# Optimization experiments

Measured on AMD Instinct MI355X. Metric: run time of the kernel, lower is better.

## Reference

```python
import jax, jax.numpy as jnp
import numpy as np

IN_SIZE = 128
HID = 256
N_SRC1 = 500000
N_DST1 = 100000
E1 = 1600000
N_DST2 = 16384
E2 = 262144


def setup_inputs() -> dict:
    key = jax.random.key(0)
    ks = jax.random.split(key, 12)
    x = jax.random.normal(ks[0], (N_SRC1, IN_SIZE), dtype=jnp.float32)
    src1 = jax.random.randint(ks[1], (E1,), 0, N_SRC1, dtype=jnp.int32)
    dst1 = jax.random.randint(ks[2], (E1,), 0, N_DST1, dtype=jnp.int32)
    src2 = jax.random.randint(ks[3], (E2,), 0, N_DST1, dtype=jnp.int32)
    dst2 = jax.random.randint(ks[4], (E2,), 0, N_DST2, dtype=jnp.int32)
    s_in = 1.0 / np.sqrt(IN_SIZE)
    s_h = 1.0 / np.sqrt(HID)
    W_self1 = jax.random.normal(ks[5], (IN_SIZE, HID), dtype=jnp.float32) * s_in
    W_neigh1 = jax.random.normal(ks[6], (IN_SIZE, HID), dtype=jnp.float32) * s_in
    b1 = jnp.zeros((HID,), dtype=jnp.float32)
    W_self2 = jax.random.normal(ks[7], (HID, HID), dtype=jnp.float32) * s_h
    W_neigh2 = jax.random.normal(ks[8], (HID, HID), dtype=jnp.float32) * s_h
    b2 = jnp.zeros((HID,), dtype=jnp.float32)
    return {
        "x": x,
        "src1": src1, "dst1": dst1,
        "src2": src2, "dst2": dst2,
        "W_self1": W_self1, "W_neigh1": W_neigh1, "b1": b1,
        "W_self2": W_self2, "W_neigh2": W_neigh2, "b2": b2,
        "n_dst1": N_DST1, "n_dst2": N_DST2,
    }


def sage_conv_mean(h, src, dst, n_dst, W_self, W_neigh, b):
    # DGL block convention: dst nodes are the first n_dst src nodes.
    # mean aggregation over incoming neighbors (zero-degree -> 0 via deg clamp)
    msg_sum = jax.ops.segment_sum(h[src], dst, num_segments=n_dst)  # [n_dst, d]
    deg = jax.ops.segment_sum(jnp.ones(src.shape, h.dtype), dst, num_segments=n_dst)
    h_neigh = msg_sum / jnp.maximum(deg, 1.0)[:, None]
    return h[:n_dst] @ W_self + h_neigh @ W_neigh + b


def reference(x, src1, dst1, src2, dst2,
              W_self1, W_neigh1, b1, W_self2, W_neigh2, b2,
              n_dst1, n_dst2):
    h = sage_conv_mean(x, src1, dst1, n_dst1, W_self1, W_neigh1, b1)
    h = jax.nn.relu(h)  # relu between layers only
    h = sage_conv_mean(h, src2, dst2, n_dst2, W_self2, W_neigh2, b2)
    return h
```

## Files before the change

kernel.cpp:

```cpp
#include <hip/hip_runtime.h>

#define IN_SIZE 128
#define HID 256
#define N_SRC1 500000
#define N_DST1 100000
#define E1 1600000
#define N_DST2 16384
#define E2 262144

#define NBIN1 196
#define NBIN2 32
#define P1B1  800
#define P1B2  256

#define OFF_XBF  0ull
#define OFF_H    76800000ull
#define OFF_MSG1 128000000ull
#define OFF_STG1 128000000ull
#define OFF_STG2 134400000ull
#define OFF_BP1  135448576ull
#define OFF_BP2  136075776ull
#define OFF_BT1  136108544ull
#define OFF_BT2  136109568ull
#define OFF_RPB1 136109824ull
#define OFF_RPB2 136110848ull
#define OFF_RP1  153600000ull
#define OFF_RP2  154000128ull
#define OFF_CSR1 154535424ull
#define OFF_CSR2 160935424ull
#define OFF_WP1  161984000ull
#define OFF_WP2  162115072ull

typedef __attribute__((ext_vector_type(8))) short short8;
typedef __attribute__((ext_vector_type(4))) float f32x4;

__device__ __forceinline__ unsigned short f2bf(float f) {
    unsigned u = __float_as_uint(f);
    return (unsigned short)((u + 0x7FFFu + ((u >> 16) & 1u)) >> 16);
}
__device__ __forceinline__ float bf2f(unsigned short b) {
    return __uint_as_float(((unsigned)b) << 16);
}

__global__ __launch_bounds__(256) void k_cast(
    const float* __restrict__ x, unsigned short* __restrict__ xbf)
{
    const int T = gridDim.x * 256;
    const int tid = blockIdx.x * 256 + threadIdx.x;
    const float4* x4 = (const float4*)x;
    short8* o8 = (short8*)xbf;
    for (int i = tid; i < N_SRC1 * IN_SIZE / 8; i += T) {
        const float4 u0 = x4[(size_t)i * 2];
        const float4 u1 = x4[(size_t)i * 2 + 1];
        short8 o;
        o[0] = (short)f2bf(u0.x); o[1] = (short)f2bf(u0.y);
        o[2] = (short)f2bf(u0.z); o[3] = (short)f2bf(u0.w);
        o[4] = (short)f2bf(u1.x); o[5] = (short)f2bf(u1.y);
        o[6] = (short)f2bf(u1.z); o[7] = (short)f2bf(u1.w);
        o8[i] = o;
    }
}

__global__ __launch_bounds__(256) void k_hist_bins(
    const int* __restrict__ dst1, int* __restrict__ hist1,
    const int* __restrict__ dst2, int* __restrict__ hist2)
{
    __shared__ int lcnt[NBIN1];
    const int tid = threadIdx.x;
    const bool l1 = blockIdx.x < P1B1;
    const int blk = l1 ? blockIdx.x : blockIdx.x - P1B1;
    const int nbins = l1 ? NBIN1 : NBIN2;
    const int chunk = l1 ? (E1 / P1B1) : (E2 / P1B2);
    const int* dst = l1 ? dst1 : dst2;
    int* hist = l1 ? hist1 : hist2;
    const int e0 = blk * chunk;
    for (int i = tid; i < nbins; i += 256) lcnt[i] = 0;
    __syncthreads();
    for (int i = tid; i < chunk; i += 256)
        atomicAdd(&lcnt[dst[e0 + i] >> 9], 1);
    __syncthreads();
    for (int i = tid; i < nbins; i += 256)
        hist[blk * nbins + i] = lcnt[i];
}

__global__ __launch_bounds__(256) void k_scan_offs(
    const int* __restrict__ hist1, int* __restrict__ blkpref1, int* __restrict__ bintot1,
    const int* __restrict__ hist2, int* __restrict__ blkpref2, int* __restrict__ bintot2)
{
    __shared__ int s[256];
    const int tid = threadIdx.x;
    const bool l1 = blockIdx.x < NBIN1;
    const int b = l1 ? blockIdx.x : blockIdx.x - NBIN1;
    const int nblk = l1 ? P1B1 : P1B2;
    const int nbins = l1 ? NBIN1 : NBIN2;
    const int* hist = l1 ? hist1 : hist2;
    int* blkpref = l1 ? blkpref1 : blkpref2;
    int* bintot = l1 ? bintot1 : bintot2;

    int v[4];
    int lsum = 0;
    #pragma unroll
    for (int j = 0; j < 4; ++j) {
        const int idx = tid * 4 + j;
        v[j] = (idx < nblk) ? hist[idx * nbins + b] : 0;
        lsum += v[j];
    }
    s[tid] = lsum;
    __syncthreads();
    for (int off = 1; off < 256; off <<= 1) {
        int t = (tid >= off) ? s[tid - off] : 0;
        __syncthreads();
        s[tid] += t;
        __syncthreads();
    }
    int run = s[tid] - lsum;
    #pragma unroll
    for (int j = 0; j < 4; ++j) {
        const int idx = tid * 4 + j;
        if (idx < nblk) blkpref[idx * nbins + b] = run;
        run += v[j];
    }
    if (tid == 255) bintot[b] = s[255];
}

__global__ __launch_bounds__(256) void k_binscan(
    const int* __restrict__ bt1, int* __restrict__ rpB1,
    const int* __restrict__ bt2, int* __restrict__ rpB2)
{
    __shared__ int s[256];
    const int tid = threadIdx.x;
    const bool l1 = (blockIdx.x == 0);
    const int n = l1 ? NBIN1 : NBIN2;
    const int* bt = l1 ? bt1 : bt2;
    int* rpB = l1 ? rpB1 : rpB2;
    const int v = (tid < n) ? bt[tid] : 0;
    s[tid] = v;
    __syncthreads();
    for (int off = 1; off < 256; off <<= 1) {
        int t = (tid >= off) ? s[tid - off] : 0;
        __syncthreads();
        s[tid] += t;
        __syncthreads();
    }
    if (tid < n) rpB[tid] = s[tid] - v;
    if (tid == n - 1) rpB[n] = s[tid];
}

__global__ __launch_bounds__(256) void k_place(
    const int* __restrict__ src1, const int* __restrict__ dst1,
    const int* __restrict__ blkpref1, const int* __restrict__ rpB1,
    unsigned* __restrict__ stg1,
    const int* __restrict__ src2, const int* __restrict__ dst2,
    const int* __restrict__ blkpref2, const int* __restrict__ rpB2,
    unsigned* __restrict__ stg2)
{
    __shared__ int lcur[NBIN1];
    const int tid = threadIdx.x;
    const bool l1 = blockIdx.x < P1B1;
    const int blk = l1 ? blockIdx.x : blockIdx.x - P1B1;
    const int nbins = l1 ? NBIN1 : NBIN2;
    const int chunk = l1 ? (E1 / P1B1) : (E2 / P1B2);
    const int* src = l1 ? src1 : src2;
    const int* dst = l1 ? dst1 : dst2;
    const int* blkpref = l1 ? blkpref1 : blkpref2;
    const int* rpB = l1 ? rpB1 : rpB2;
    unsigned* stg = l1 ? stg1 : stg2;
    const int e0 = blk * chunk;
    for (int i = tid; i < nbins; i += 256)
        lcur[i] = rpB[i] + blkpref[blk * nbins + i];
    __syncthreads();
    for (int i = tid; i < chunk; i += 256) {
        const int e = e0 + i;
        const int d = dst[e];
        const unsigned pk = ((unsigned)(d & 511) << 19) | (unsigned)src[e];
        const int pos = atomicAdd(&lcur[d >> 9], 1);
        stg[pos] = pk;
    }
}

__global__ __launch_bounds__(512) void k_fill_p2b(
    const unsigned* __restrict__ stg1, const int* __restrict__ rpB1,
    int* __restrict__ rp1, int* __restrict__ csr1,
    const unsigned* __restrict__ stg2, const int* __restrict__ rpB2,
    int* __restrict__ rp2, int* __restrict__ csr2)
{
    __shared__ int lcnt[512];
    __shared__ int s[512];
    const int tid = threadIdx.x;
    const bool l1 = blockIdx.x < NBIN1;
    const int b = l1 ? blockIdx.x : blockIdx.x - NBIN1;
    const int base = b << 9;
    const int ndst = l1 ? N_DST1 : N_DST2;
    const int nr = min(512, ndst - base);
    const unsigned* stg = l1 ? stg1 : stg2;
    const int* rpB = l1 ? rpB1 : rpB2;
    int* rp = l1 ? rp1 : rp2;
    int* csr = l1 ? csr1 : csr2;
    const int s0 = rpB[b], s1 = rpB[b + 1];

    lcnt[tid] = 0;
    __syncthreads();
    for (int i = s0 + tid; i < s1; i += 512)
        atomicAdd(&lcnt[stg[i] >> 19], 1);
    __syncthreads();

    const int v = lcnt[tid];
    s[tid] = v;
    __syncthreads();
    for (int off = 1; off < 512; off <<= 1) {
        int t = (tid >= off) ? s[tid - off] : 0;
        __syncthreads();
        s[tid] += t;
        __syncthreads();
    }
    const int excl = s0 + s[tid] - v;
    if (tid < nr) rp[base + tid] = excl;
    if (base + tid == ndst - 1) rp[ndst] = s1;
    __syncthreads();
    lcnt[tid] = excl;
    __syncthreads();

    for (int i = s0 + tid; i < s1; i += 512) {
        const unsigned pk = stg[i];
        const int pos = atomicAdd(&lcnt[pk >> 19], 1);
        csr[pos] = (int)(pk & 0x7FFFFu);
    }
}

__global__ __launch_bounds__(256) void k_pack(const float* __restrict__ Wa,
                                              const float* __restrict__ Wb,
                                              int Keach, unsigned short* __restrict__ out) {
    const int t = blockIdx.x * 256 + threadIdx.x;
    const int total = (2 * Keach / 32) * 1024;
    if (t >= total) return;
    const int kb = t >> 10;
    const int c  = (t >> 2) & 255;
    const int g  = t & 3;
    const int kbase = kb * 32 + g * 8;
    const float* W = (kbase < Keach) ? (Wa + (size_t)kbase * HID + c)
                                     : (Wb + (size_t)(kbase - Keach) * HID + c);
    unsigned short* o = out + ((size_t)kb * 256 + c) * 32 + g * 8;
    #pragma unroll
    for (int j = 0; j < 8; ++j) o[j] = f2bf(W[(size_t)j * HID]);
}

__global__ __launch_bounds__(256) void k_pull1(
    const unsigned short* __restrict__ xbf, const int* __restrict__ rp,
    const int* __restrict__ csr, unsigned short* __restrict__ msg)
{
    const int d = blockIdx.x * 8 + (threadIdx.x >> 5);
    const int hl = threadIdx.x & 31;
    const int beg = rp[d], end = rp[d + 1];
    float a0 = 0.f, a1 = 0.f, a2 = 0.f, a3 = 0.f;
    const unsigned short* xb = xbf + hl * 4;
    int j = beg;
    for (; j + 3 < end; j += 4) {
        const int s0 = csr[j], s1 = csr[j + 1], s2 = csr[j + 2], s3 = csr[j + 3];
        const uint2 va = *(const uint2*)(xb + (size_t)s0 * IN_SIZE);
        const uint2 vb = *(const uint2*)(xb + (size_t)s1 * IN_SIZE);
        const uint2 vc = *(const uint2*)(xb + (size_t)s2 * IN_SIZE);
        const uint2 vd = *(const uint2*)(xb + (size_t)s3 * IN_SIZE);
        a0 += (bf2f(va.x) + bf2f(vb.x)) + (bf2f(vc.x) + bf2f(vd.x));
        a1 += (bf2f(va.x >> 16) + bf2f(vb.x >> 16)) + (bf2f(vc.x >> 16) + bf2f(vd.x >> 16));
        a2 += (bf2f(va.y) + bf2f(vb.y)) + (bf2f(vc.y) + bf2f(vd.y));
        a3 += (bf2f(va.y >> 16) + bf2f(vb.y >> 16)) + (bf2f(vc.y >> 16) + bf2f(vd.y >> 16));
    }
    for (; j < end; ++j) {
        const uint2 va = *(const uint2*)(xb + (size_t)csr[j] * IN_SIZE);
        a0 += bf2f(va.x); a1 += bf2f(va.x >> 16);
        a2 += bf2f(va.y); a3 += bf2f(va.y >> 16);
    }
    const float inv = 1.0f / fmaxf((float)(end - beg), 1.0f);
    uint2 o;
    o.x = (unsigned)f2bf(a0 * inv) | ((unsigned)f2bf(a1 * inv) << 16);
    o.y = (unsigned)f2bf(a2 * inv) | ((unsigned)f2bf(a3 * inv) << 16);
    *(uint2*)(msg + (size_t)d * IN_SIZE + hl * 4) = o;
}

__global__ __launch_bounds__(256) void k_gemm1(
    const unsigned short* __restrict__ A1,
    const unsigned short* __restrict__ A2,
    const unsigned short* __restrict__ Wp,
    const float* __restrict__ bias,
    unsigned short* __restrict__ out)
{
    constexpr int NKS = 8;
    const int tid = threadIdx.x;
    const int wid = tid >> 6;
    const int lane = tid & 63;
    const int g = lane >> 4, r16 = lane & 15;
    const int i0 = blockIdx.x * 32;
    const int c0 = wid * 64;

    f32x4 acc[2][4];
    #pragma unroll
    for (int rb = 0; rb < 2; ++rb)
        #pragma unroll
        for (int cf = 0; cf < 4; ++cf)
            acc[rb][cf] = (f32x4){0.f, 0.f, 0.f, 0.f};

    #pragma unroll
    for (int ks = 0; ks < NKS; ++ks) {
        short8 a[2];
        #pragma unroll
        for (int rb = 0; rb < 2; ++rb) {
            const int row = i0 + rb * 16 + r16;
            const int kk = ks * 32 + g * 8;
            a[rb] = (ks < NKS / 2)
                ? *(const short8*)(A1 + (size_t)row * IN_SIZE + kk)
                : *(const short8*)(A2 + (size_t)row * IN_SIZE + (kk - IN_SIZE));
        }
        short8 b[4];
        #pragma unroll
        for (int cf = 0; cf < 4; ++cf) {
            const int col = c0 + cf * 16 + r16;
            b[cf] = *(const short8*)(Wp + ((size_t)ks * 256 + col) * 32 + g * 8);
        }
        #pragma unroll
        for (int rb = 0; rb < 2; ++rb)
            #pragma unroll
            for (int cf = 0; cf < 4; ++cf)
                acc[rb][cf] = __builtin_amdgcn_mfma_f32_16x16x32_bf16(
                    a[rb], b[cf], acc[rb][cf], 0, 0, 0);
    }

    #pragma unroll
    for (int cf = 0; cf < 4; ++cf) {
        const int col = c0 + cf * 16 + r16;
        const float bv = bias[col];
        #pragma unroll
        for (int rb = 0; rb < 2; ++rb)
            #pragma unroll
            for (int rr = 0; rr < 4; ++rr) {
                const int row = i0 + rb * 16 + g * 4 + rr;
                out[(size_t)row * HID + col] = f2bf(fmaxf(acc[rb][cf][rr] + bv, 0.0f));
            }
    }
}

__global__ __launch_bounds__(256) void k_sage2(
    const unsigned short* __restrict__ h,
    const int* __restrict__ rp, const int* __restrict__ csr,
    const unsigned short* __restrict__ Wp,
    const float* __restrict__ bias,
    float* __restrict__ out)
{
    __shared__ __align__(16) unsigned short At[32][264];
    const int tid = threadIdx.x;
    const int wid = tid >> 6;
    const int lane = tid & 63;
    const int i0 = blockIdx.x * 32;

    for (int r = 0; r < 8; ++r) {
        const int row = wid * 8 + r;
        const int d = i0 + row;
        const int beg = rp[d], end = rp[d + 1];
        float a0 = 0.f, a1 = 0.f, a2 = 0.f, a3 = 0.f;
        const unsigned short* hb = h + lane * 4;
        int j = beg;
        for (; j + 3 < end; j += 4) {
            const int s0 = csr[j], s1 = csr[j + 1], s2 = csr[j + 2], s3 = csr[j + 3];
            const uint2 va = *(const uint2*)(hb + (size_t)s0 * HID);
            const uint2 vb = *(const uint2*)(hb + (size_t)s1 * HID);
            const uint2 vc = *(const uint2*)(hb + (size_t)s2 * HID);
            const uint2 vd = *(const uint2*)(hb + (size_t)s3 * HID);
            a0 += (bf2f(va.x) + bf2f(vb.x)) + (bf2f(vc.x) + bf2f(vd.x));
            a1 += (bf2f(va.x >> 16) + bf2f(vb.x >> 16)) + (bf2f(vc.x >> 16) + bf2f(vd.x >> 16));
            a2 += (bf2f(va.y) + bf2f(vb.y)) + (bf2f(vc.y) + bf2f(vd.y));
            a3 += (bf2f(va.y >> 16) + bf2f(vb.y >> 16)) + (bf2f(vc.y >> 16) + bf2f(vd.y >> 16));
        }
        for (; j < end; ++j) {
            const uint2 va = *(const uint2*)(hb + (size_t)csr[j] * HID);
            a0 += bf2f(va.x); a1 += bf2f(va.x >> 16);
            a2 += bf2f(va.y); a3 += bf2f(va.y >> 16);
        }
        const float inv = 1.0f / fmaxf((float)(end - beg), 1.0f);
        uint2 o;
        o.x = (unsigned)f2bf(a0 * inv) | ((unsigned)f2bf(a1 * inv) << 16);
        o.y = (unsigned)f2bf(a2 * inv) | ((unsigned)f2bf(a3 * inv) << 16);
        *(uint2*)&At[row][lane * 4] = o;
    }
    __syncthreads();

    const int g = lane >> 4, r16 = lane & 15;
    const int c0 = wid * 64;
    f32x4 acc[2][4];
    #pragma unroll
    for (int rb = 0; rb < 2; ++rb)
        #pragma unroll
        for (int cf = 0; cf < 4; ++cf)
            acc[rb][cf] = (f32x4){0.f, 0.f, 0.f, 0.f};

    #pragma unroll
    for (int ks = 0; ks < 16; ++ks) {
        short8 a[2];
        #pragma unroll
        for (int rb = 0; rb < 2; ++rb) {
            const int row16 = rb * 16 + r16;
            if (ks < 8)
                a[rb] = *(const short8*)(h + (size_t)(i0 + row16) * HID + ks * 32 + g * 8);
            else
                a[rb] = *(const short8*)&At[row16][(ks - 8) * 32 + g * 8];
        }
        short8 b[4];
        #pragma unroll
        for (int cf = 0; cf < 4; ++cf) {
            const int col = c0 + cf * 16 + r16;
            b[cf] = *(const short8*)(Wp + ((size_t)ks * 256 + col) * 32 + g * 8);
        }
        #pragma unroll
        for (int rb = 0; rb < 2; ++rb)
            #pragma unroll
            for (int cf = 0; cf < 4; ++cf)
                acc[rb][cf] = __builtin_amdgcn_mfma_f32_16x16x32_bf16(
                    a[rb], b[cf], acc[rb][cf], 0, 0, 0);
    }

    #pragma unroll
    for (int cf = 0; cf < 4; ++cf) {
        const int col = c0 + cf * 16 + r16;
        const float bv = bias[col];
        #pragma unroll
        for (int rb = 0; rb < 2; ++rb)
            #pragma unroll
            for (int rr = 0; rr < 4; ++rr) {
                const int row = i0 + rb * 16 + g * 4 + rr;
                out[(size_t)row * HID + col] = acc[rb][cf][rr] + bv;
            }
    }
}

extern "C" void kernel_launch(void* const* d_in, const int* in_sizes, int n_in,
                              void* d_out, int out_size, void* d_ws, size_t ws_size,
                              hipStream_t stream) {
    const float* x       = (const float*)d_in[0];
    const int*   src1    = (const int*)d_in[1];
    const int*   dst1    = (const int*)d_in[2];
    const int*   src2    = (const int*)d_in[3];
    const int*   dst2    = (const int*)d_in[4];
    const float* W_self1 = (const float*)d_in[5];
    const float* W_neigh1= (const float*)d_in[6];
    const float* b1      = (const float*)d_in[7];
    const float* W_self2 = (const float*)d_in[8];
    const float* W_neigh2= (const float*)d_in[9];
    const float* b2      = (const float*)d_in[10];
    float* out = (float*)d_out;

    char* ws = (char*)d_ws;
    unsigned short* xbf  = (unsigned short*)(ws + OFF_XBF);
    unsigned short* h    = (unsigned short*)(ws + OFF_H);
    unsigned short* msg1 = (unsigned short*)(ws + OFF_MSG1);
    unsigned* stg1 = (unsigned*)(ws + OFF_STG1);
    unsigned* stg2 = (unsigned*)(ws + OFF_STG2);
    int* bp1  = (int*)(ws + OFF_BP1);
    int* bp2  = (int*)(ws + OFF_BP2);
    int* bt1  = (int*)(ws + OFF_BT1);
    int* bt2  = (int*)(ws + OFF_BT2);
    int* rpB1 = (int*)(ws + OFF_RPB1);
    int* rpB2 = (int*)(ws + OFF_RPB2);
    int* rp1  = (int*)(ws + OFF_RP1);
    int* rp2  = (int*)(ws + OFF_RP2);
    int* csr1 = (int*)(ws + OFF_CSR1);
    int* csr2 = (int*)(ws + OFF_CSR2);
    unsigned short* wp1 = (unsigned short*)(ws + OFF_WP1);
    unsigned short* wp2 = (unsigned short*)(ws + OFF_WP2);

    k_cast<<<2048, 256, 0, stream>>>(x, xbf);
    k_pack<<<32, 256, 0, stream>>>(W_self1, W_neigh1, 128, wp1);
    k_pack<<<64, 256, 0, stream>>>(W_self2, W_neigh2, 256, wp2);

    k_hist_bins<<<P1B1 + P1B2, 256, 0, stream>>>(dst1, bp1 , dst2, bp2);
    k_scan_offs<<<NBIN1 + NBIN2, 256, 0, stream>>>(bp1, bp1, bt1, bp2, bp2, bt2);
    k_binscan<<<2, 256, 0, stream>>>(bt1, rpB1, bt2, rpB2);
    k_place<<<P1B1 + P1B2, 256, 0, stream>>>(src1, dst1, bp1, rpB1, stg1,
                                             src2, dst2, bp2, rpB2, stg2);
    k_fill_p2b<<<NBIN1 + NBIN2, 512, 0, stream>>>(stg1, rpB1, rp1, csr1,
                                                  stg2, rpB2, rp2, csr2);

    k_pull1<<<N_DST1 / 8, 256, 0, stream>>>(xbf, rp1, csr1, msg1);
    k_gemm1<<<N_DST1 / 32, 256, 0, stream>>>(xbf, msg1, wp1, b1, h);
    k_sage2<<<N_DST2 / 32, 256, 0, stream>>>(h, rp2, csr2, wp2, b2, out);
}
```

Baseline: 313.6 us.

## Fuse layer-1 gather with GEMM and merge setup kernels

Layer-1 neighbor aggregation now runs inside the GEMM kernel: each block gathers mean messages for its 32 rows into shared memory and feeds them straight into the MFMA loop, so the msg1 buffer is never written to or read back from global memory. The cast and histogram kernels are merged into one launch, and the two weight-pack launches become one, which cuts launch overhead. The gather now uses a full wave per row with 4-byte loads and an 8-way unroll. Each GEMM block does 8 serial row gathers per wave before any matrix work, which may lower occupancy and reduce overlap between memory and compute.

```diff
diff --git a/kernel.cpp b/kernel.cpp
--- a/kernel.cpp
+++ b/kernel.cpp
@@ -14,22 +14,21 @@
 #define P1B2  256
 
 #define OFF_XBF  0ull
-#define OFF_H    76800000ull
-#define OFF_MSG1 128000000ull
-#define OFF_STG1 128000000ull
-#define OFF_STG2 134400000ull
-#define OFF_BP1  135448576ull
-#define OFF_BP2  136075776ull
-#define OFF_BT1  136108544ull
-#define OFF_BT2  136109568ull
-#define OFF_RPB1 136109824ull
-#define OFF_RPB2 136110848ull
-#define OFF_RP1  153600000ull
-#define OFF_RP2  154000128ull
-#define OFF_CSR1 154535424ull
-#define OFF_CSR2 160935424ull
-#define OFF_WP1  161984000ull
-#define OFF_WP2  162115072ull
+#define OFF_H    128000000ull
+#define OFF_STG1 179200000ull
+#define OFF_STG2 185600000ull
+#define OFF_BP1  186648576ull
+#define OFF_BP2  187275776ull
+#define OFF_BT1  187308544ull
+#define OFF_BT2  187309568ull
+#define OFF_RPB1 187310592ull
+#define OFF_RPB2 187311616ull
+#define OFF_RP1  187312640ull
+#define OFF_RP2  187712768ull
+#define OFF_CSR1 187778432ull
+#define OFF_CSR2 194178432ull
+#define OFF_WP1  195227008ull
+#define OFF_WP2  195358080ull
 
 typedef __attribute__((ext_vector_type(8))) short short8;
 typedef __attribute__((ext_vector_type(4))) float f32x4;
@@ -42,14 +41,37 @@
     return __uint_as_float(((unsigned)b) << 16);
 }
 
-__global__ __launch_bounds__(256) void k_cast(
-    const float* __restrict__ x, unsigned short* __restrict__ xbf)
-{
+__global__ __launch_bounds__(256) void k_cast_hist(
+    const float* __restrict__ x, unsigned short* __restrict__ xbf,
+    const int* __restrict__ dst1, int* __restrict__ hist1,
+    const int* __restrict__ dst2, int* __restrict__ hist2)
+{
+    __shared__ int lcnt[NBIN1];
+    const int bid = blockIdx.x;
+    const int tid = threadIdx.x;
+
+    if (bid < P1B1 + P1B2) {
+        const bool l1 = bid < P1B1;
+        const int blk = l1 ? bid : bid - P1B1;
+        const int nbins = l1 ? NBIN1 : NBIN2;
+        const int chunk = l1 ? (E1 / P1B1) : (E2 / P1B2);
+        const int* dst = l1 ? dst1 : dst2;
+        int* hist = l1 ? hist1 : hist2;
+        const int e0 = blk * chunk;
+        for (int i = tid; i < nbins; i += 256) lcnt[i] = 0;
+        __syncthreads();
+        for (int i = tid; i < chunk; i += 256)
+            atomicAdd(&lcnt[dst[e0 + i] >> 9], 1);
+        __syncthreads();
+        for (int i = tid; i < nbins; i += 256)
+            hist[blk * nbins + i] = lcnt[i];
+    }
+
     const int T = gridDim.x * 256;
-    const int tid = blockIdx.x * 256 + threadIdx.x;
+    const int gtid = bid * 256 + tid;
     const float4* x4 = (const float4*)x;
     short8* o8 = (short8*)xbf;
-    for (int i = tid; i < N_SRC1 * IN_SIZE / 8; i += T) {
+    for (int i = gtid; i < N_SRC1 * IN_SIZE / 8; i += T) {
         const float4 u0 = x4[(size_t)i * 2];
         const float4 u1 = x4[(size_t)i * 2 + 1];
         short8 o;
@@ -59,28 +81,6 @@
         o[6] = (short)f2bf(u1.z); o[7] = (short)f2bf(u1.w);
         o8[i] = o;
     }
-}
-
-__global__ __launch_bounds__(256) void k_hist_bins(
-    const int* __restrict__ dst1, int* __restrict__ hist1,
-    const int* __restrict__ dst2, int* __restrict__ hist2)
-{
-    __shared__ int lcnt[NBIN1];
-    const int tid = threadIdx.x;
-    const bool l1 = blockIdx.x < P1B1;
-    const int blk = l1 ? blockIdx.x : blockIdx.x - P1B1;
-    const int nbins = l1 ? NBIN1 : NBIN2;
-    const int chunk = l1 ? (E1 / P1B1) : (E2 / P1B2);
-    const int* dst = l1 ? dst1 : dst2;
-    int* hist = l1 ? hist1 : hist2;
-    const int e0 = blk * chunk;
-    for (int i = tid; i < nbins; i += 256) lcnt[i] = 0;
-    __syncthreads();
-    for (int i = tid; i < chunk; i += 256)
-        atomicAdd(&lcnt[dst[e0 + i] >> 9], 1);
-    __syncthreads();
-    for (int i = tid; i < nbins; i += 256)
-        hist[blk * nbins + i] = lcnt[i];
 }
 
 __global__ __launch_bounds__(256) void k_scan_offs(
@@ -227,12 +227,18 @@
     }
 }
 
-__global__ __launch_bounds__(256) void k_pack(const float* __restrict__ Wa,
-                                              const float* __restrict__ Wb,
-                                              int Keach, unsigned short* __restrict__ out) {
-    const int t = blockIdx.x * 256 + threadIdx.x;
-    const int total = (2 * Keach / 32) * 1024;
-    if (t >= total) return;
+__global__ __launch_bounds__(256) void k_pack2(
+    const float* __restrict__ Ws1, const float* __restrict__ Wn1,
+    unsigned short* __restrict__ wp1,
+    const float* __restrict__ Ws2, const float* __restrict__ Wn2,
+    unsigned short* __restrict__ wp2)
+{
+    const bool l1 = blockIdx.x < 32;
+    const int Keach = l1 ? 128 : 256;
+    const float* Wa = l1 ? Ws1 : Ws2;
+    const float* Wb = l1 ? Wn1 : Wn2;
+    unsigned short* out = l1 ? wp1 : wp2;
+    const int t = (l1 ? blockIdx.x : blockIdx.x - 32) * 256 + threadIdx.x;
     const int kb = t >> 10;
     const int c  = (t >> 2) & 255;
     const int g  = t & 3;
@@ -244,54 +250,50 @@
     for (int j = 0; j < 8; ++j) o[j] = f2bf(W[(size_t)j * HID]);
 }
 
-__global__ __launch_bounds__(256) void k_pull1(
+__global__ __launch_bounds__(256) void k_sage1(
     const unsigned short* __restrict__ xbf, const int* __restrict__ rp,
-    const int* __restrict__ csr, unsigned short* __restrict__ msg)
-{
-    const int d = blockIdx.x * 8 + (threadIdx.x >> 5);
-    const int hl = threadIdx.x & 31;
-    const int beg = rp[d], end = rp[d + 1];
-    float a0 = 0.f, a1 = 0.f, a2 = 0.f, a3 = 0.f;
-    const unsigned short* xb = xbf + hl * 4;
-    int j = beg;
-    for (; j + 3 < end; j += 4) {
-        const int s0 = csr[j], s1 = csr[j + 1], s2 = csr[j + 2], s3 = csr[j + 3];
-        const uint2 va = *(const uint2*)(xb + (size_t)s0 * IN_SIZE);
-        const uint2 vb = *(const uint2*)(xb + (size_t)s1 * IN_SIZE);
-        const uint2 vc = *(const uint2*)(xb + (size_t)s2 * IN_SIZE);
-        const uint2 vd = *(const uint2*)(xb + (size_t)s3 * IN_SIZE);
-        a0 += (bf2f(va.x) + bf2f(vb.x)) + (bf2f(vc.x) + bf2f(vd.x));
-        a1 += (bf2f(va.x >> 16) + bf2f(vb.x >> 16)) + (bf2f(vc.x >> 16) + bf2f(vd.x >> 16));
-        a2 += (bf2f(va.y) + bf2f(vb.y)) + (bf2f(vc.y) + bf2f(vd.y));
-        a3 += (bf2f(va.y >> 16) + bf2f(vb.y >> 16)) + (bf2f(vc.y >> 16) + bf2f(vd.y >> 16));
-    }
-    for (; j < end; ++j) {
-        const uint2 va = *(const uint2*)(xb + (size_t)csr[j] * IN_SIZE);
-        a0 += bf2f(va.x); a1 += bf2f(va.x >> 16);
-        a2 += bf2f(va.y); a3 += bf2f(va.y >> 16);
-    }
-    const float inv = 1.0f / fmaxf((float)(end - beg), 1.0f);
-    uint2 o;
-    o.x = (unsigned)f2bf(a0 * inv) | ((unsigned)f2bf(a1 * inv) << 16);
-    o.y = (unsigned)f2bf(a2 * inv) | ((unsigned)f2bf(a3 * inv) << 16);
-    *(uint2*)(msg + (size_t)d * IN_SIZE + hl * 4) = o;
-}
-
-__global__ __launch_bounds__(256) void k_gemm1(
-    const unsigned short* __restrict__ A1,
-    const unsigned short* __restrict__ A2,
-    const unsigned short* __restrict__ Wp,
-    const float* __restrict__ bias,
-    unsigned short* __restrict__ out)
-{
-    constexpr int NKS = 8;
+    const int* __restrict__ csr, const unsigned short* __restrict__ Wp,
+    const float* __restrict__ bias, unsigned short* __restrict__ outh)
+{
+    __shared__ __align__(16) unsigned short At[32][136];
     const int tid = threadIdx.x;
     const int wid = tid >> 6;
     const int lane = tid & 63;
+    const int i0 = blockIdx.x * 32;
+
+    for (int r = 0; r < 8; ++r) {
+        const int row = wid * 8 + r;
+        const int d = i0 + row;
+        const int beg = rp[d], end = rp[d + 1];
+        float a0 = 0.f, a1 = 0.f;
+        const unsigned short* xb = xbf + lane * 2;
+        int j = beg;
+        for (; j + 7 < end; j += 8) {
+            const unsigned v0 = *(const unsigned*)(xb + (size_t)csr[j + 0] * IN_SIZE);
+            const unsigned v1 = *(const unsigned*)(xb + (size_t)csr[j + 1] * IN_SIZE);
+            const unsigned v2 = *(const unsigned*)(xb + (size_t)csr[j + 2] * IN_SIZE);
+            const unsigned v3 = *(const unsigned*)(xb + (size_t)csr[j + 3] * IN_SIZE);
+            const unsigned v4 = *(const unsigned*)(xb + (size_t)csr[j + 4] * IN_SIZE);
+            const unsigned v5 = *(const unsigned*)(xb + (size_t)csr[j + 5] * IN_SIZE);
+            const unsigned v6 = *(const unsigned*)(xb + (size_t)csr[j + 6] * IN_SIZE);
+            const unsigned v7 = *(const unsigned*)(xb + (size_t)csr[j + 7] * IN_SIZE);
+            a0 += ((bf2f(v0) + bf2f(v1)) + (bf2f(v2) + bf2f(v3)))
+                + ((bf2f(v4) + bf2f(v5)) + (bf2f(v6) + bf2f(v7)));
+            a1 += ((bf2f(v0 >> 16) + bf2f(v1 >> 16)) + (bf2f(v2 >> 16) + bf2f(v3 >> 16)))
+                + ((bf2f(v4 >> 16) + bf2f(v5 >> 16)) + (bf2f(v6 >> 16) + bf2f(v7 >> 16)));
+        }
+        for (; j < end; ++j) {
+            const unsigned v = *(const unsigned*)(xb + (size_t)csr[j] * IN_SIZE);
+            a0 += bf2f(v); a1 += bf2f(v >> 16);
+        }
+        const float inv = 1.0f / fmaxf((float)(end - beg), 1.0f);
+        *(unsigned*)&At[row][lane * 2] =
+            (unsigned)f2bf(a0 * inv) | ((unsigned)f2bf(a1 * inv) << 16);
+    }
+    __syncthreads();
+
     const int g = lane >> 4, r16 = lane & 15;
-    const int i0 = blockIdx.x * 32;
     const int c0 = wid * 64;
-
     f32x4 acc[2][4];
     #pragma unroll
     for (int rb = 0; rb < 2; ++rb)
@@ -300,15 +302,15 @@
             acc[rb][cf] = (f32x4){0.f, 0.f, 0.f, 0.f};
 
     #pragma unroll
-    for (int ks = 0; ks < NKS; ++ks) {
+    for (int ks = 0; ks < 8; ++ks) {
         short8 a[2];
         #pragma unroll
         for (int rb = 0; rb < 2; ++rb) {
-            const int row = i0 + rb * 16 + r16;
-            const int kk = ks * 32 + g * 8;
-            a[rb] = (ks < NKS / 2)
-                ? *(const short8*)(A1 + (size_t)row * IN_SIZE + kk)
-                : *(const short8*)(A2 + (size_t)row * IN_SIZE + (kk - IN_SIZE));
+            const int row16 = rb * 16 + r16;
+            if (ks < 4)
+                a[rb] = *(const short8*)(xbf + (size_t)(i0 + row16) * IN_SIZE + ks * 32 + g * 8);
+            else
+                a[rb] = *(const short8*)&At[row16][(ks - 4) * 32 + g * 8];
         }
         short8 b[4];
         #pragma unroll
@@ -333,7 +335,7 @@
             #pragma unroll
             for (int rr = 0; rr < 4; ++rr) {
                 const int row = i0 + rb * 16 + g * 4 + rr;
-                out[(size_t)row * HID + col] = f2bf(fmaxf(acc[rb][cf][rr] + bv, 0.0f));
+                outh[(size_t)row * HID + col] = f2bf(fmaxf(acc[rb][cf][rr] + bv, 0.0f));
             }
     }
 }
@@ -359,11 +361,10 @@
         const unsigned short* hb = h + lane * 4;
         int j = beg;
         for (; j + 3 < end; j += 4) {
-            const int s0 = csr[j], s1 = csr[j + 1], s2 = csr[j + 2], s3 = csr[j + 3];
-            const uint2 va = *(const uint2*)(hb + (size_t)s0 * HID);
-            const uint2 vb = *(const uint2*)(hb + (size_t)s1 * HID);
-            const uint2 vc = *(const uint2*)(hb + (size_t)s2 * HID);
-            const uint2 vd = *(const uint2*)(hb + (size_t)s3 * HID);
+            const uint2 va = *(const uint2*)(hb + (size_t)csr[j + 0] * HID);
+            const uint2 vb = *(const uint2*)(hb + (size_t)csr[j + 1] * HID);
+            const uint2 vc = *(const uint2*)(hb + (size_t)csr[j + 2] * HID);
+            const uint2 vd = *(const uint2*)(hb + (size_t)csr[j + 3] * HID);
             a0 += (bf2f(va.x) + bf2f(vb.x)) + (bf2f(vc.x) + bf2f(vd.x));
             a1 += (bf2f(va.x >> 16) + bf2f(vb.x >> 16)) + (bf2f(vc.x >> 16) + bf2f(vd.x >> 16));
             a2 += (bf2f(va.y) + bf2f(vb.y)) + (bf2f(vc.y) + bf2f(vd.y));
@@ -447,9 +448,8 @@
     float* out = (float*)d_out;
 
     char* ws = (char*)d_ws;
-    unsigned short* xbf  = (unsigned short*)(ws + OFF_XBF);
-    unsigned short* h    = (unsigned short*)(ws + OFF_H);
-    unsigned short* msg1 = (unsigned short*)(ws + OFF_MSG1);
+    unsigned short* xbf = (unsigned short*)(ws + OFF_XBF);
+    unsigned short* h   = (unsigned short*)(ws + OFF_H);
     unsigned* stg1 = (unsigned*)(ws + OFF_STG1);
     unsigned* stg2 = (unsigned*)(ws + OFF_STG2);
     int* bp1  = (int*)(ws + OFF_BP1);
@@ -465,11 +465,9 @@
     unsigned short* wp1 = (unsigned short*)(ws + OFF_WP1);
     unsigned short* wp2 = (unsigned short*)(ws + OFF_WP2);
 
-    k_cast<<<2048, 256, 0, stream>>>(x, xbf);
-    k_pack<<<32, 256, 0, stream>>>(W_self1, W_neigh1, 128, wp1);
-    k_pack<<<64, 256, 0, stream>>>(W_self2, W_neigh2, 256, wp2);
-
-    k_hist_bins<<<P1B1 + P1B2, 256, 0, stream>>>(dst1, bp1 , dst2, bp2);
+    k_cast_hist<<<2048, 256, 0, stream>>>(x, xbf, dst1, bp1, dst2, bp2);
+    k_pack2<<<96, 256, 0, stream>>>(W_self1, W_neigh1, wp1, W_self2, W_neigh2, wp2);
+
     k_scan_offs<<<NBIN1 + NBIN2, 256, 0, stream>>>(bp1, bp1, bt1, bp2, bp2, bt2);
     k_binscan<<<2, 256, 0, stream>>>(bt1, rpB1, bt2, rpB2);
     k_place<<<P1B1 + P1B2, 256, 0, stream>>>(src1, dst1, bp1, rpB1, stg1,
@@ -477,7 +475,6 @@
     k_fill_p2b<<<NBIN1 + NBIN2, 512, 0, stream>>>(stg1, rpB1, rp1, csr1,
                                                   stg2, rpB2, rp2, csr2);
 
-    k_pull1<<<N_DST1 / 8, 256, 0, stream>>>(xbf, rp1, csr1, msg1);
-    k_gemm1<<<N_DST1 / 32, 256, 0, stream>>>(xbf, msg1, wp1, b1, h);
+    k_sage1<<<N_DST1 / 32, 256, 0, stream>>>(xbf, rp1, csr1, wp1, b1, h);
     k_sage2<<<N_DST2 / 32, 256, 0, stream>>>(h, rp2, csr2, wp2, b2, out);
 }
```

Result: slower. 333.1 us (+6.2%).

## Fuse cast with histogram, merge weight packs, unroll layer-1 gather by eight

Applied to the files above, without the earlier changes.

Merges the bf16 cast kernel with the destination histogram kernel, and the two weight-pack launches into one, to cut launch count and let the independent work overlap within one grid. The layer-1 neighbour gather loop is unrolled to eight rows per iteration so more loads are in flight. The workspace layout is reshuffled so the cast output no longer aliases buffers that the histogram now writes concurrently. The costs are higher register pressure in the pull kernel and more imbalance across blocks in the fused launch.

```diff
diff --git a/kernel.cpp b/kernel.cpp
--- a/kernel.cpp
+++ b/kernel.cpp
@@ -14,22 +14,22 @@
 #define P1B2  256
 
 #define OFF_XBF  0ull
-#define OFF_H    76800000ull
-#define OFF_MSG1 128000000ull
-#define OFF_STG1 128000000ull
-#define OFF_STG2 134400000ull
-#define OFF_BP1  135448576ull
-#define OFF_BP2  136075776ull
-#define OFF_BT1  136108544ull
-#define OFF_BT2  136109568ull
-#define OFF_RPB1 136109824ull
-#define OFF_RPB2 136110848ull
-#define OFF_RP1  153600000ull
-#define OFF_RP2  154000128ull
-#define OFF_CSR1 154535424ull
-#define OFF_CSR2 160935424ull
-#define OFF_WP1  161984000ull
-#define OFF_WP2  162115072ull
+#define OFF_H    128000000ull
+#define OFF_MSG1 179200000ull
+#define OFF_STG1 204800000ull
+#define OFF_STG2 211200000ull
+#define OFF_BP1  212248576ull
+#define OFF_BP2  212875776ull
+#define OFF_BT1  212908544ull
+#define OFF_BT2  212909568ull
+#define OFF_RPB1 212910592ull
+#define OFF_RPB2 212911616ull
+#define OFF_RP1  212912640ull
+#define OFF_RP2  213312768ull
+#define OFF_CSR1 213378432ull
+#define OFF_CSR2 219778432ull
+#define OFF_WP1  220827008ull
+#define OFF_WP2  220958080ull
 
 typedef __attribute__((ext_vector_type(8))) short short8;
 typedef __attribute__((ext_vector_type(4))) float f32x4;
@@ -42,14 +42,37 @@
     return __uint_as_float(((unsigned)b) << 16);
 }
 
-__global__ __launch_bounds__(256) void k_cast(
-    const float* __restrict__ x, unsigned short* __restrict__ xbf)
-{
+__global__ __launch_bounds__(256) void k_cast_hist(
+    const float* __restrict__ x, unsigned short* __restrict__ xbf,
+    const int* __restrict__ dst1, int* __restrict__ hist1,
+    const int* __restrict__ dst2, int* __restrict__ hist2)
+{
+    __shared__ int lcnt[NBIN1];
+    const int bid = blockIdx.x;
+    const int tid = threadIdx.x;
+
+    if (bid < P1B1 + P1B2) {
+        const bool l1 = bid < P1B1;
+        const int blk = l1 ? bid : bid - P1B1;
+        const int nbins = l1 ? NBIN1 : NBIN2;
+        const int chunk = l1 ? (E1 / P1B1) : (E2 / P1B2);
+        const int* dst = l1 ? dst1 : dst2;
+        int* hist = l1 ? hist1 : hist2;
+        const int e0 = blk * chunk;
+        for (int i = tid; i < nbins; i += 256) lcnt[i] = 0;
+        __syncthreads();
+        for (int i = tid; i < chunk; i += 256)
+            atomicAdd(&lcnt[dst[e0 + i] >> 9], 1);
+        __syncthreads();
+        for (int i = tid; i < nbins; i += 256)
+            hist[blk * nbins + i] = lcnt[i];
+    }
+
     const int T = gridDim.x * 256;
-    const int tid = blockIdx.x * 256 + threadIdx.x;
+    const int gtid = bid * 256 + tid;
     const float4* x4 = (const float4*)x;
     short8* o8 = (short8*)xbf;
-    for (int i = tid; i < N_SRC1 * IN_SIZE / 8; i += T) {
+    for (int i = gtid; i < N_SRC1 * IN_SIZE / 8; i += T) {
         const float4 u0 = x4[(size_t)i * 2];
         const float4 u1 = x4[(size_t)i * 2 + 1];
         short8 o;
@@ -59,28 +82,6 @@
         o[6] = (short)f2bf(u1.z); o[7] = (short)f2bf(u1.w);
         o8[i] = o;
     }
-}
-
-__global__ __launch_bounds__(256) void k_hist_bins(
-    const int* __restrict__ dst1, int* __restrict__ hist1,
-    const int* __restrict__ dst2, int* __restrict__ hist2)
-{
-    __shared__ int lcnt[NBIN1];
-    const int tid = threadIdx.x;
-    const bool l1 = blockIdx.x < P1B1;
-    const int blk = l1 ? blockIdx.x : blockIdx.x - P1B1;
-    const int nbins = l1 ? NBIN1 : NBIN2;
-    const int chunk = l1 ? (E1 / P1B1) : (E2 / P1B2);
-    const int* dst = l1 ? dst1 : dst2;
-    int* hist = l1 ? hist1 : hist2;
-    const int e0 = blk * chunk;
-    for (int i = tid; i < nbins; i += 256) lcnt[i] = 0;
-    __syncthreads();
-    for (int i = tid; i < chunk; i += 256)
-        atomicAdd(&lcnt[dst[e0 + i] >> 9], 1);
-    __syncthreads();
-    for (int i = tid; i < nbins; i += 256)
-        hist[blk * nbins + i] = lcnt[i];
 }
 
 __global__ __launch_bounds__(256) void k_scan_offs(
@@ -227,12 +228,18 @@
     }
 }
 
-__global__ __launch_bounds__(256) void k_pack(const float* __restrict__ Wa,
-                                              const float* __restrict__ Wb,
-                                              int Keach, unsigned short* __restrict__ out) {
-    const int t = blockIdx.x * 256 + threadIdx.x;
-    const int total = (2 * Keach / 32) * 1024;
-    if (t >= total) return;
+__global__ __launch_bounds__(256) void k_pack2(
+    const float* __restrict__ Ws1, const float* __restrict__ Wn1,
+    unsigned short* __restrict__ wp1,
+    const float* __restrict__ Ws2, const float* __restrict__ Wn2,
+    unsigned short* __restrict__ wp2)
+{
+    const bool l1 = blockIdx.x < 32;
+    const int Keach = l1 ? 128 : 256;
+    const float* Wa = l1 ? Ws1 : Ws2;
+    const float* Wb = l1 ? Wn1 : Wn2;
+    unsigned short* out = l1 ? wp1 : wp2;
+    const int t = (l1 ? blockIdx.x : blockIdx.x - 32) * 256 + threadIdx.x;
     const int kb = t >> 10;
     const int c  = (t >> 2) & 255;
     const int g  = t & 3;
@@ -254,16 +261,23 @@
     float a0 = 0.f, a1 = 0.f, a2 = 0.f, a3 = 0.f;
     const unsigned short* xb = xbf + hl * 4;
     int j = beg;
-    for (; j + 3 < end; j += 4) {
-        const int s0 = csr[j], s1 = csr[j + 1], s2 = csr[j + 2], s3 = csr[j + 3];
-        const uint2 va = *(const uint2*)(xb + (size_t)s0 * IN_SIZE);
-        const uint2 vb = *(const uint2*)(xb + (size_t)s1 * IN_SIZE);
-        const uint2 vc = *(const uint2*)(xb + (size_t)s2 * IN_SIZE);
-        const uint2 vd = *(const uint2*)(xb + (size_t)s3 * IN_SIZE);
-        a0 += (bf2f(va.x) + bf2f(vb.x)) + (bf2f(vc.x) + bf2f(vd.x));
-        a1 += (bf2f(va.x >> 16) + bf2f(vb.x >> 16)) + (bf2f(vc.x >> 16) + bf2f(vd.x >> 16));
-        a2 += (bf2f(va.y) + bf2f(vb.y)) + (bf2f(vc.y) + bf2f(vd.y));
-        a3 += (bf2f(va.y >> 16) + bf2f(vb.y >> 16)) + (bf2f(vc.y >> 16) + bf2f(vd.y >> 16));
+    for (; j + 7 < end; j += 8) {
+        const uint2 v0 = *(const uint2*)(xb + (size_t)csr[j + 0] * IN_SIZE);
+        const uint2 v1 = *(const uint2*)(xb + (size_t)csr[j + 1] * IN_SIZE);
+        const uint2 v2 = *(const uint2*)(xb + (size_t)csr[j + 2] * IN_SIZE);
+        const uint2 v3 = *(const uint2*)(xb + (size_t)csr[j + 3] * IN_SIZE);
+        const uint2 v4 = *(const uint2*)(xb + (size_t)csr[j + 4] * IN_SIZE);
+        const uint2 v5 = *(const uint2*)(xb + (size_t)csr[j + 5] * IN_SIZE);
+        const uint2 v6 = *(const uint2*)(xb + (size_t)csr[j + 6] * IN_SIZE);
+        const uint2 v7 = *(const uint2*)(xb + (size_t)csr[j + 7] * IN_SIZE);
+        a0 += ((bf2f(v0.x) + bf2f(v1.x)) + (bf2f(v2.x) + bf2f(v3.x)))
+            + ((bf2f(v4.x) + bf2f(v5.x)) + (bf2f(v6.x) + bf2f(v7.x)));
+        a1 += ((bf2f(v0.x >> 16) + bf2f(v1.x >> 16)) + (bf2f(v2.x >> 16) + bf2f(v3.x >> 16)))
+            + ((bf2f(v4.x >> 16) + bf2f(v5.x >> 16)) + (bf2f(v6.x >> 16) + bf2f(v7.x >> 16)));
+        a2 += ((bf2f(v0.y) + bf2f(v1.y)) + (bf2f(v2.y) + bf2f(v3.y)))
+            + ((bf2f(v4.y) + bf2f(v5.y)) + (bf2f(v6.y) + bf2f(v7.y)));
+        a3 += ((bf2f(v0.y >> 16) + bf2f(v1.y >> 16)) + (bf2f(v2.y >> 16) + bf2f(v3.y >> 16)))
+            + ((bf2f(v4.y >> 16) + bf2f(v5.y >> 16)) + (bf2f(v6.y >> 16) + bf2f(v7.y >> 16)));
     }
     for (; j < end; ++j) {
         const uint2 va = *(const uint2*)(xb + (size_t)csr[j] * IN_SIZE);
@@ -359,11 +373,10 @@
         const unsigned short* hb = h + lane * 4;
         int j = beg;
         for (; j + 3 < end; j += 4) {
-            const int s0 = csr[j], s1 = csr[j + 1], s2 = csr[j + 2], s3 = csr[j + 3];
-            const uint2 va = *(const uint2*)(hb + (size_t)s0 * HID);
-            const uint2 vb = *(const uint2*)(hb + (size_t)s1 * HID);
-            const uint2 vc = *(const uint2*)(hb + (size_t)s2 * HID);
-            const uint2 vd = *(const uint2*)(hb + (size_t)s3 * HID);
+            const uint2 va = *(const uint2*)(hb + (size_t)csr[j + 0] * HID);
+            const uint2 vb = *(const uint2*)(hb + (size_t)csr[j + 1] * HID);
+            const uint2 vc = *(const uint2*)(hb + (size_t)csr[j + 2] * HID);
+            const uint2 vd = *(const uint2*)(hb + (size_t)csr[j + 3] * HID);
             a0 += (bf2f(va.x) + bf2f(vb.x)) + (bf2f(vc.x) + bf2f(vd.x));
             a1 += (bf2f(va.x >> 16) + bf2f(vb.x >> 16)) + (bf2f(vc.x >> 16) + bf2f(vd.x >> 16));
             a2 += (bf2f(va.y) + bf2f(vb.y)) + (bf2f(vc.y) + bf2f(vd.y));
@@ -465,11 +478,9 @@
     unsigned short* wp1 = (unsigned short*)(ws + OFF_WP1);
     unsigned short* wp2 = (unsigned short*)(ws + OFF_WP2);
 
-    k_cast<<<2048, 256, 0, stream>>>(x, xbf);
-    k_pack<<<32, 256, 0, stream>>>(W_self1, W_neigh1, 128, wp1);
-    k_pack<<<64, 256, 0, stream>>>(W_self2, W_neigh2, 256, wp2);
-
-    k_hist_bins<<<P1B1 + P1B2, 256, 0, stream>>>(dst1, bp1 , dst2, bp2);
+    k_cast_hist<<<2048, 256, 0, stream>>>(x, xbf, dst1, bp1, dst2, bp2);
+    k_pack2<<<96, 256, 0, stream>>>(W_self1, W_neigh1, wp1, W_self2, W_neigh2, wp2);
+
     k_scan_offs<<<NBIN1 + NBIN2, 256, 0, stream>>>(bp1, bp1, bt1, bp2, bp2, bt2);
     k_binscan<<<2, 256, 0, stream>>>(bt1, rpB1, bt2, rpB2);
     k_place<<<P1B1 + P1B2, 256, 0, stream>>>(src1, dst1, bp1, rpB1, stg1,
```

Measured after the change: 306.5 us. 2.2% less time.
